# Kernel optimization log

Hardware: AMD Instinct MI355X
Metric: run time of the kernel (lower is better)

Reference implementation:

```python
import jax, jax.numpy as jnp
import numpy as np

D = 512
DB = D // 4          # 128
R = 4                # window radius
KB = 9               # boundary kernel
DH = D // 2          # attn mlp hidden
VOCABS = {"quality": 64, "root": 13, "bass": 13, "key": 25}
COMPS = ["quality", "root", "bass", "key"]
B, T = 4, 4096


def _ln(x, g, b, eps=1e-5):
    mu = jnp.mean(x, axis=-1, keepdims=True)
    var = jnp.var(x, axis=-1, keepdims=True)
    return (x - mu) * jax.lax.rsqrt(var + eps) * g + b


def setup_inputs() -> dict:
    key = jax.random.key(0)
    ks = jax.random.split(key, 24)
    s = 0.02
    inp = {
        "h": jax.random.normal(ks[0], (B, T, D), jnp.float32),
        # boundary head
        "w_bnd": jax.random.normal(ks[1], (D,), jnp.float32) * s,
        "b_bnd": jnp.zeros((1,), jnp.float32),
        # boundary smoother conv1d(1,1,KB)
        "conv_k": jax.random.normal(ks[2], (KB,), jnp.float32) * s,
        "conv_b": jnp.zeros((1,), jnp.float32),
        # FiLM boundary embeddings
        "e0": jnp.zeros((DB,), jnp.float32),
        "e1": jax.random.normal(ks[3], (DB,), jnp.float32) * s,
        # LayerNorms
        "ln_in_g": jnp.ones((D + DB,), jnp.float32),
        "ln_in_b": jnp.zeros((D + DB,), jnp.float32),
        "ln_h_g": jnp.ones((D,), jnp.float32),
        "ln_h_b": jnp.zeros((D,), jnp.float32),
        # FiLM mlp
        "film_w": jax.random.normal(ks[4], (D + DB, 2 * D), jnp.float32) * s,
        "film_b": jnp.zeros((2 * D,), jnp.float32),
        # per-component attn MLP (stacked over 4 comps)
        "attn_w1": jax.random.normal(ks[5], (4, D, DH), jnp.float32) * s,
        "attn_b1": jnp.zeros((4, DH), jnp.float32),
        "attn_w2": jax.random.normal(ks[6], (4, DH), jnp.float32) * s,
        "attn_b2": jnp.zeros((4,), jnp.float32),
        # per-component projector first layer (stacked)
        "proj_w1": jax.random.normal(ks[7], (4, D, D), jnp.float32) * s,
        "proj_b1": jnp.zeros((4, D), jnp.float32),
    }
    for i, c in enumerate(COMPS):
        inp[f"proj_w2_{c[0]}" if c != "key" else "proj_w2_k"] = jax.random.normal(ks[8 + i], (D, VOCABS[c]), jnp.float32) * s
        inp[f"proj_b2_{c[0]}" if c != "key" else "proj_b2_k"] = jnp.zeros((VOCABS[c],), jnp.float32)
    return inp


def reference(h, w_bnd, b_bnd, conv_k, conv_b, e0, e1,
              ln_in_g, ln_in_b, ln_h_g, ln_h_b, film_w, film_b,
              attn_w1, attn_b1, attn_w2, attn_b2, proj_w1, proj_b1,
              proj_w2_q, proj_b2_q, proj_w2_r, proj_b2_r,
              proj_w2_b, proj_b2_b, proj_w2_k, proj_b2_k):
    Bz, Tz, Dz = h.shape
    # boundary head + smoothing (conv1d, same padding) + sigmoid
    bl = jnp.einsum("btd,d->bt", h, w_bnd) + b_bnd[0]            # [B,T]
    sm = jax.lax.conv_general_dilated(bl[:, None, :], conv_k[None, None, :],
                                      (1,), [(KB // 2, KB // 2)]) + conv_b[0]
    b_soft = jax.nn.sigmoid(sm[:, 0, :])                          # [B,T]
    # FiLM
    eb = b_soft[..., None] * e1 + (1.0 - b_soft[..., None]) * e0  # [B,T,DB]
    film_in = _ln(jnp.concatenate([h, eb], axis=-1), ln_in_g, ln_in_b)
    gb = film_in @ film_w + film_b                                # [B,T,2D]
    gamma, beta = gb[..., :Dz], gb[..., Dz:]
    z = _ln(h, ln_h_g, ln_h_b) * (1.0 + gamma) + beta             # [B,T,D]
    # local windows via replicate pad + gather
    hp = jnp.pad(h, ((0, 0), (R, R), (0, 0)), mode="edge")        # [B,T+2R,D]
    idx = jnp.arange(Tz)[:, None] + jnp.arange(2 * R + 1)[None, :]  # [T,W]
    local = hp[:, idx, :]                                         # [B,T,W,D]
    c = jnp.concatenate([z[:, :, None, :], local], axis=2)        # [B,T,C,D]
    # attention pooling for all 4 components at once
    s1 = jax.nn.gelu(jnp.einsum("btcd,kdh->kbtch", c, attn_w1)
                     + attn_b1[:, None, None, None, :], approximate=False)
    scores = jnp.einsum("kbtch,kh->kbtc", s1, attn_w2) + attn_b2[:, None, None, None]
    attn = jax.nn.softmax(scores, axis=-1)                        # [K,B,T,C]
    pooled = jnp.einsum("kbtc,btcd->kbtd", attn, c)               # [K,B,T,D]
    p1 = jax.nn.gelu(jnp.einsum("kbtd,kde->kbte", pooled, proj_w1)
                     + proj_b1[:, None, None, :], approximate=False)
    lq = p1[0] @ proj_w2_q + proj_b2_q
    lr = p1[1] @ proj_w2_r + proj_b2_r
    lb = p1[2] @ proj_w2_b + proj_b2_b
    lk = p1[3] @ proj_w2_k + proj_b2_k
    return jnp.concatenate([lq, lr, lb, lk, bl[..., None]], axis=-1)  # [B,T,116]
```

## Files before the change

kernel.cpp:

```cpp
#include <hip/hip_runtime.h>
#include <hip/hip_bf16.h>

typedef unsigned short u16;
typedef unsigned int u32;

#define NR 16384
#define TT 4096

typedef __bf16 bf16_t;
typedef bf16_t bf16x8 __attribute__((ext_vector_type(8)));
typedef float f32x4 __attribute__((ext_vector_type(4)));

__device__ __forceinline__ float b2f(u16 u){ return __uint_as_float(((u32)u)<<16); }
__device__ __forceinline__ u16 f2b(float f){
  u32 u = __float_as_uint(f);
  u32 r = u + 0x7fffu + ((u>>16)&1u);
  return (u16)(r>>16);
}
__device__ __forceinline__ void up2(u32 u, float&a, float&b){
  a = __uint_as_float(u<<16);
  b = __uint_as_float(u & 0xffff0000u);
}
__device__ __forceinline__ void ld8(const u16* p, float* f){
  uint4 v = *(const uint4*)p;
  up2(v.x,f[0],f[1]); up2(v.y,f[2],f[3]);
  up2(v.z,f[4],f[5]); up2(v.w,f[6],f[7]);
}
__device__ __forceinline__ float wred(float v){
  #pragma unroll
  for(int o=32;o>0;o>>=1) v += __shfl_down(v,o,64);
  return v;
}
__device__ __forceinline__ float gelu_f(float x){
  return 0.5f*x*(1.0f+erff(x*0.7071067811865475f));
}
__device__ __forceinline__ void gl_lds(const void* g, void* l){
  __builtin_amdgcn_global_load_lds(
      (__attribute__((address_space(1))) void*)(void*)g,
      (__attribute__((address_space(3))) void*)l, 16, 0, 0);
}

__global__ void k_tw(const float* __restrict__ src, u16* __restrict__ dst,
                     int K, int N, long long sS, long long sD){
  __shared__ float t[32][33];
  const float* S = src + (size_t)blockIdx.z*sS;
  u16* D = dst + (size_t)blockIdx.z*sD;
  int k0 = blockIdx.y*32, n0 = blockIdx.x*32;
  int r = threadIdx.x>>5, c = threadIdx.x&31;
  #pragma unroll
  for(int p=0;p<4;p++) t[r+p*8][c] = S[(size_t)(k0+r+p*8)*N + n0 + c];
  __syncthreads();
  #pragma unroll
  for(int p=0;p<4;p++) D[(size_t)(n0+r+p*8)*K + k0 + c] = f2b(t[c][r+p*8]);
}

__global__ void k_w2c(const float* __restrict__ wq, const float* __restrict__ bq,
                      const float* __restrict__ wr, const float* __restrict__ br,
                      const float* __restrict__ wb_, const float* __restrict__ bb_,
                      const float* __restrict__ wk, const float* __restrict__ bk,
                      u16* __restrict__ W2c, float* __restrict__ b2c){
  int idx = blockIdx.x;
  int p = idx>>5, j = idx&31, tid = threadIdx.x;
  const float* Wm; const float* Bm; int V; int cofs = 0;
  if(p<=1){ Wm=wq; Bm=bq; V=64; cofs = p*32; }
  else if(p==2){ Wm=wr; Bm=br; V=13; }
  else if(p==3){ Wm=wb_; Bm=bb_; V=13; }
  else { Wm=wk; Bm=bk; V=25; }
  int c = j + cofs;
  bool valid = c < V;
  for(int k=tid;k<512;k+=256)
    W2c[(size_t)idx*512 + k] = f2b(valid ? Wm[(size_t)k*V + c] : 0.f);
  if(tid==0) b2c[idx] = valid ? Bm[c] : 0.f;
}

__global__ void k_bnd(const float* __restrict__ h, const float* __restrict__ wb,
                      const float* __restrict__ bb,
                      float* __restrict__ bl, float* __restrict__ hsum, float* __restrict__ hss,
                      u16* __restrict__ hbf, float* __restrict__ out){
  int wave = threadIdx.x>>6, lane = threadIdx.x&63;
  int n = blockIdx.x*4 + wave;
  const float4* hp = (const float4*)(h + (size_t)n*512 + lane*8);
  const float4* wp = (const float4*)(wb + lane*8);
  float4 h0 = hp[0], h1 = hp[1], w0 = wp[0], w1 = wp[1];
  float hv[8] = {h0.x,h0.y,h0.z,h0.w,h1.x,h1.y,h1.z,h1.w};
  float wv[8] = {w0.x,w0.y,w0.z,w0.w,w1.x,w1.y,w1.z,w1.w};
  float dot=0.f, s=0.f, ss=0.f;
  #pragma unroll
  for(int i=0;i<8;i++){ dot += hv[i]*wv[i]; s += hv[i]; ss += hv[i]*hv[i]; }
  u16* hd = hbf + (size_t)n*512 + lane*8;
  *(ushort4*)hd     = make_ushort4(f2b(hv[0]),f2b(hv[1]),f2b(hv[2]),f2b(hv[3]));
  *(ushort4*)(hd+4) = make_ushort4(f2b(hv[4]),f2b(hv[5]),f2b(hv[6]),f2b(hv[7]));
  dot = wred(dot); s = wred(s); ss = wred(ss);
  if(lane==0){
    float v = dot + bb[0];
    bl[n] = v; hsum[n]=s; hss[n]=ss;
    out[(size_t)n*116 + 115] = v;
  }
}

__global__ void k_conv(const float* __restrict__ bl, const float* __restrict__ ck,
                       const float* __restrict__ cb, float* __restrict__ bsoft){
  int n = blockIdx.x*256 + threadIdx.x;
  int b = n>>12, t = n&4095;
  float acc = cb[0];
  #pragma unroll
  for(int i=0;i<9;i++){
    int tt = t-4+i;
    if(tt>=0 && tt<TT) acc += bl[(b<<12)+tt]*ck[i];
  }
  bsoft[n] = 1.0f/(1.0f+expf(-acc));
}

__global__ void k_filmin(const float* __restrict__ h, const float* __restrict__ bsoft,
                         const float* __restrict__ e0, const float* __restrict__ e1,
                         const float* __restrict__ g, const float* __restrict__ bb,
                         u16* __restrict__ fin){
  __shared__ float xb[640];
  __shared__ float red[8];
  int n = blockIdx.x, tid = threadIdx.x;
  float bs = bsoft[n];
  float s=0.f, ss=0.f;
  for(int idx=tid; idx<640; idx+=256){
    float v;
    if(idx<512) v = h[(size_t)n*512+idx];
    else { int j=idx-512; v = bs*e1[j] + (1.0f-bs)*e0[j]; }
    xb[idx]=v; s+=v; ss+=v*v;
  }
  s = wred(s); ss = wred(ss);
  int wave = tid>>6, lane = tid&63;
  if(lane==0){ red[wave]=s; red[wave+4]=ss; }
  __syncthreads();
  float S = red[0]+red[1]+red[2]+red[3];
  float SS = red[4]+red[5]+red[6]+red[7];
  float mu = S*(1.0f/640.0f);
  float var = SS*(1.0f/640.0f) - mu*mu;
  float rs = rsqrtf(var + 1e-5f);
  for(int idx=tid; idx<640; idx+=256){
    float v = (xb[idx]-mu)*rs*g[idx] + bb[idx];
    fin[(size_t)n*640+idx] = f2b(v);
  }
}

template<int ACT>
__global__ __launch_bounds__(256) void k_mgemm(
    const u16* __restrict__ X, const u16* __restrict__ WT, const float* __restrict__ Bv,
    u16* __restrict__ C, int K, int Nc, int ldC,
    long long sX, long long sW, long long sB, long long sC){
  __shared__ __align__(16) u16 As[128*32];
  __shared__ __align__(16) u16 Bs[128*32];
  int tid = threadIdx.x;
  int wave = tid>>6, lane = tid&63;
  const u16* Xb = X + (size_t)blockIdx.z*sX;
  const u16* Wb = WT + (size_t)blockIdx.z*sW;
  const float* Bb = Bv + (size_t)blockIdx.z*sB;
  u16* Cb = C + (size_t)blockIdx.z*sC;
  int row0 = blockIdx.y*128, col0 = blockIdx.x*128;
  int wr = (wave>>1)*64, wc = (wave&1)*64;
  int lrow = lane>>2;
  int lcol = (lane&3)*8;
  int m15 = lane&15, q = lane>>4;
  f32x4 acc[4][4] = {};
  for(int k0=0;k0<K;k0+=32){
    const u16* ga = Xb + (size_t)(row0 + wave*32 + lrow)*K + k0 + lcol;
    u16* la = As + wave*32*32;
    gl_lds(ga, la);
    gl_lds(ga + (size_t)16*K, la + 16*32);
    const u16* gw = Wb + (size_t)(col0 + wave*32 + lrow)*K + k0 + lcol;
    u16* lb = Bs + wave*32*32;
    gl_lds(gw, lb);
    gl_lds(gw + (size_t)16*K, lb + 16*32);
    __syncthreads();
    bf16x8 af[4], bfr[4];
    #pragma unroll
    for(int i=0;i<4;i++){
      af[i]  = *(const bf16x8*)&As[(wr + i*16 + m15)*32 + q*8];
      bfr[i] = *(const bf16x8*)&Bs[(wc + i*16 + m15)*32 + q*8];
    }
    #pragma unroll
    for(int i=0;i<4;i++)
      #pragma unroll
      for(int j=0;j<4;j++)
        acc[i][j] = __builtin_amdgcn_mfma_f32_16x16x32_bf16(bfr[j], af[i], acc[i][j], 0,0,0);
    __syncthreads();
  }
  #pragma unroll
  for(int i=0;i<4;i++){
    size_t mrow = (size_t)(row0 + wr + i*16 + m15)*ldC;
    #pragma unroll
    for(int j=0;j<4;j++){
      int n0 = col0 + wc + j*16 + q*4;
      float4 bias = *(const float4*)&Bb[n0];
      float v0 = acc[i][j][0] + bias.x;
      float v1 = acc[i][j][1] + bias.y;
      float v2 = acc[i][j][2] + bias.z;
      float v3 = acc[i][j][3] + bias.w;
      if(ACT){ v0=gelu_f(v0); v1=gelu_f(v1); v2=gelu_f(v2); v3=gelu_f(v3); }
      *(ushort4*)(Cb + mrow + n0) = make_ushort4(f2b(v0),f2b(v1),f2b(v2),f2b(v3));
    }
  }
}

__global__ __launch_bounds__(256) void k_f2(
    const u16* __restrict__ X2, const u16* __restrict__ W2c, const float* __restrict__ b2c,
    float* __restrict__ out){
  __shared__ __align__(16) u16 As[128*32];
  __shared__ __align__(16) u16 Bs[32*32];
  int tid = threadIdx.x, wave = tid>>6, lane = tid&63;
  int row0 = blockIdx.x*128, p = blockIdx.y;
  int hk = (p<=1)?0:(p-1);
  int B0 = (p==0)?0:(p==1)?32:(p==2)?64:(p==3)?77:90;
  int V  = (p<=1)?32:(p==4)?25:13;
  int lrow = lane>>2, lcol = (lane&3)*8, m15 = lane&15, q = lane>>4;
  f32x4 acc[2][2] = {};
  for(int k0=0;k0<512;k0+=32){
    const u16* ga = X2 + (size_t)(row0 + wave*32 + lrow)*2048 + hk*512 + k0 + lcol;
    u16* la = As + wave*32*32;
    gl_lds(ga, la);
    gl_lds(ga + (size_t)16*2048, la + 16*32);
    if(wave<2){
      const u16* gw = W2c + (size_t)(p*32 + wave*16 + lrow)*512 + k0 + lcol;
      gl_lds(gw, Bs + wave*16*32);
    }
    __syncthreads();
    bf16x8 af[2], bfr[2];
    #pragma unroll
    for(int i=0;i<2;i++) af[i] = *(const bf16x8*)&As[(wave*32 + i*16 + m15)*32 + q*8];
    #pragma unroll
    for(int j=0;j<2;j++) bfr[j] = *(const bf16x8*)&Bs[(j*16+m15)*32 + q*8];
    #pragma unroll
    for(int i=0;i<2;i++)
      #pragma unroll
      for(int j=0;j<2;j++)
        acc[i][j] = __builtin_amdgcn_mfma_f32_16x16x32_bf16(bfr[j], af[i], acc[i][j], 0,0,0);
    __syncthreads();
  }
  #pragma unroll
  for(int i=0;i<2;i++){
    size_t mrow = (size_t)(row0 + wave*32 + i*16 + m15)*116;
    #pragma unroll
    for(int j=0;j<2;j++){
      int nl0 = j*16 + q*4;
      #pragma unroll
      for(int r=0;r<4;r++){
        int nl = nl0 + r;
        if(nl < V) out[mrow + B0 + nl] = acc[i][j][r] + b2c[p*32+nl];
      }
    }
  }
}

__global__ void k_z(const float* __restrict__ h, const float* __restrict__ hsum,
                    const float* __restrict__ hss, const float* __restrict__ g,
                    const float* __restrict__ bb, const u16* __restrict__ gb,
                    u16* __restrict__ z){
  int n = blockIdx.x, tid = threadIdx.x;
  float mu = hsum[n]*(1.0f/512.0f);
  float var = hss[n]*(1.0f/512.0f) - mu*mu;
  float rs = rsqrtf(var+1e-5f);
  for(int idx=tid; idx<512; idx+=256){
    float hv = h[(size_t)n*512+idx];
    float ln = (hv-mu)*rs*g[idx]+bb[idx];
    float gamma = b2f(gb[(size_t)n*1024+idx]);
    float beta  = b2f(gb[(size_t)n*1024+512+idx]);
    z[(size_t)n*512+idx] = f2b(ln*(1.0f+gamma)+beta);
  }
}

__global__ void k_scred(const u16* __restrict__ G, const float* __restrict__ w2,
                        const float* __restrict__ b2v, float* __restrict__ sc){
  int wave = threadIdx.x>>6, lane = threadIdx.x&63;
  int n = blockIdx.x*4 + wave;
  int k = blockIdx.y;
  uint2 gv = *(const uint2*)(G + ((size_t)k*NR + n)*256 + lane*4);
  float4 wv = *(const float4*)(w2 + k*256 + lane*4);
  float a0,a1,a2,a3;
  up2(gv.x,a0,a1); up2(gv.y,a2,a3);
  float s = a0*wv.x+a1*wv.y+a2*wv.z+a3*wv.w;
  s = wred(s);
  if(lane==0) sc[(size_t)k*NR+n] = s + b2v[k];
}

__global__ __launch_bounds__(256) void k_pool(
    const u16* __restrict__ hb, const u16* __restrict__ z,
    const float* __restrict__ sch, const float* __restrict__ scz,
    u16* __restrict__ P){
  int wave = threadIdx.x>>6, lane = threadIdx.x&63;
  int n = blockIdx.x*4 + wave;
  int b = n>>12, t = n&4095;
  int k = lane&3, j = lane>>2;
  float s;
  if(j==0) s = scz[(size_t)k*NR+n];
  else if(j<10){
    int tc = t-5+j; tc = tc<0?0:(tc>TT-1?TT-1:tc);
    s = sch[(size_t)k*NR + (b<<12) + tc];
  } else s = -1e30f;
  float m = s;
  #pragma unroll
  for(int o=4;o<64;o<<=1) m = fmaxf(m, __shfl_xor(m,o,64));
  float e = (j<10)? expf(s-m) : 0.f;
  float sum = e;
  #pragma unroll
  for(int o=4;o<64;o<<=1) sum += __shfl_xor(sum,o,64);
  float ev = e/sum;
  int d0 = lane*8;
  float acc[4][8] = {};
  #pragma unroll
  for(int jj=0;jj<10;jj++){
    const u16* src;
    if(jj==0) src = z + (size_t)n*512 + d0;
    else {
      int tc = t-5+jj; tc = tc<0?0:(tc>TT-1?TT-1:tc);
      src = hb + ((size_t)(b<<12)+tc)*512 + d0;
    }
    float f[8]; ld8(src, f);
    float w0 = __shfl(ev, jj*4+0, 64);
    float w1 = __shfl(ev, jj*4+1, 64);
    float w2 = __shfl(ev, jj*4+2, 64);
    float w3 = __shfl(ev, jj*4+3, 64);
    #pragma unroll
    for(int i=0;i<8;i++){
      acc[0][i] += w0*f[i];
      acc[1][i] += w1*f[i];
      acc[2][i] += w2*f[i];
      acc[3][i] += w3*f[i];
    }
  }
  #pragma unroll
  for(int kk=0;kk<4;kk++){
    u16* dst = P + ((size_t)kk*NR + n)*512 + d0;
    *(ushort4*)dst     = make_ushort4(f2b(acc[kk][0]),f2b(acc[kk][1]),f2b(acc[kk][2]),f2b(acc[kk][3]));
    *(ushort4*)(dst+4) = make_ushort4(f2b(acc[kk][4]),f2b(acc[kk][5]),f2b(acc[kk][6]),f2b(acc[kk][7]));
  }
}

#define OFF_BL     0u
#define OFF_BSOFT  65536u
#define OFF_HSUM   131072u
#define OFF_HSS    196608u
#define OFF_SCH    262144u
#define OFF_SCZ    524288u
#define OFF_FIN    786432u
#define OFF_GB     21757952u
#define OFF_Z      55312384u
#define OFF_HBF    72089600u
#define OFF_WF     88866816u
#define OFF_WA     90177536u
#define OFF_WP     91226112u
#define OFF_P      93323264u
#define OFF_W2C    160432128u
#define OFF_B2C    160595968u

extern "C" void kernel_launch(void* const* d_in, const int* in_sizes, int n_in,
                              void* d_out, int out_size, void* d_ws, size_t ws_size,
                              hipStream_t stream){
  const float* h       = (const float*)d_in[0];
  const float* w_bnd   = (const float*)d_in[1];
  const float* b_bnd   = (const float*)d_in[2];
  const float* conv_k  = (const float*)d_in[3];
  const float* conv_b  = (const float*)d_in[4];
  const float* e0      = (const float*)d_in[5];
  const float* e1      = (const float*)d_in[6];
  const float* ln_in_g = (const float*)d_in[7];
  const float* ln_in_b = (const float*)d_in[8];
  const float* ln_h_g  = (const float*)d_in[9];
  const float* ln_h_b  = (const float*)d_in[10];
  const float* film_w  = (const float*)d_in[11];
  const float* film_b  = (const float*)d_in[12];
  const float* attn_w1 = (const float*)d_in[13];
  const float* attn_b1 = (const float*)d_in[14];
  const float* attn_w2 = (const float*)d_in[15];
  const float* attn_b2 = (const float*)d_in[16];
  const float* proj_w1 = (const float*)d_in[17];
  const float* proj_b1 = (const float*)d_in[18];
  const float* wq = (const float*)d_in[19];
  const float* bq = (const float*)d_in[20];
  const float* wr = (const float*)d_in[21];
  const float* br = (const float*)d_in[22];
  const float* wb_ = (const float*)d_in[23];
  const float* bb_ = (const float*)d_in[24];
  const float* wk = (const float*)d_in[25];
  const float* bk = (const float*)d_in[26];
  float* out = (float*)d_out;
  char* ws = (char*)d_ws;

  float* bl    = (float*)(ws + OFF_BL);
  float* bsoft = (float*)(ws + OFF_BSOFT);
  float* hsum  = (float*)(ws + OFF_HSUM);
  float* hss   = (float*)(ws + OFF_HSS);
  float* sch   = (float*)(ws + OFF_SCH);
  float* scz   = (float*)(ws + OFF_SCZ);
  u16* fin     = (u16*)(ws + OFF_FIN);
  u16* X2      = (u16*)(ws + OFF_FIN);
  u16* gb      = (u16*)(ws + OFF_GB);
  u16* z       = (u16*)(ws + OFF_Z);
  u16* hbf     = (u16*)(ws + OFF_HBF);
  u16* wfilm   = (u16*)(ws + OFF_WF);
  u16* wattn   = (u16*)(ws + OFF_WA);
  u16* wproj   = (u16*)(ws + OFF_WP);
  u16* P       = (u16*)(ws + OFF_P);
  u16* G       = P;
  u16* w2c     = (u16*)(ws + OFF_W2C);
  float* b2c   = (float*)(ws + OFF_B2C);

  {
    dim3 g(1024/32, 640/32, 1);
    k_tw<<<g,256,0,stream>>>(film_w, wfilm, 640, 1024, 0, 0);
  }
  {
    dim3 g(256/32, 512/32, 4);
    k_tw<<<g,256,0,stream>>>(attn_w1, wattn, 512, 256, 512LL*256, 256LL*512);
  }
  {
    dim3 g(512/32, 512/32, 4);
    k_tw<<<g,256,0,stream>>>(proj_w1, wproj, 512, 512, 512LL*512, 512LL*512);
  }
  k_w2c<<<160,256,0,stream>>>(wq,bq,wr,br,wb_,bb_,wk,bk, w2c, b2c);

  k_bnd<<<NR/4,256,0,stream>>>(h,w_bnd,b_bnd,bl,hsum,hss,hbf,out);
  k_conv<<<NR/256,256,0,stream>>>(bl,conv_k,conv_b,bsoft);
  k_filmin<<<NR,256,0,stream>>>(h,bsoft,e0,e1,ln_in_g,ln_in_b,fin);

  dim3 gFilm(1024/128, NR/128, 1);
  k_mgemm<0><<<gFilm,256,0,stream>>>(fin, wfilm, film_b, gb, 640, 1024, 1024, 0,0,0,0);

  k_z<<<NR,256,0,stream>>>(h,hsum,hss,ln_h_g,ln_h_b,gb,z);

  dim3 gSc(256/128, NR/128, 4);
  dim3 gRed(NR/4, 4);
  k_mgemm<1><<<gSc,256,0,stream>>>(hbf, wattn, attn_b1, G, 512, 256, 256,
                                   0, 256LL*512, 256, (long long)NR*256);
  k_scred<<<gRed,256,0,stream>>>(G, attn_w2, attn_b2, sch);
  k_mgemm<1><<<gSc,256,0,stream>>>(z, wattn, attn_b1, G, 512, 256, 256,
                                   0, 256LL*512, 256, (long long)NR*256);
  k_scred<<<gRed,256,0,stream>>>(G, attn_w2, attn_b2, scz);

  k_pool<<<NR/4,256,0,stream>>>(hbf,z,sch,scz,P);

  dim3 gP(512/128, NR/128, 4);
  k_mgemm<1><<<gP,256,0,stream>>>(P, wproj, proj_b1, X2, 512, 512, 2048,
                                  (long long)NR*512, 512LL*512, 512, 512);

  dim3 gF(NR/128, 5);
  k_f2<<<gF,256,0,stream>>>(X2, w2c, b2c, out);
}
```

Measured before the change: 444.6 us.

## Fuse FiLM GEMM with z epilogue and attention GEMM with score reduction

The FiLM GEMM now computes gamma and beta tiles together and applies LayerNorm modulation in its epilogue to write z directly, removing the gb intermediate and the k_z kernel. The attention-MLP GEMM for h and z runs in one launch and reduces GELU times w2 into scores via atomics, eliminating the G buffer and k_scred. The projector GEMM uses a 64x256 tile, and GELU switches from erf to a tanh approximation using fast exp and rcp. The costs are atomic contention on the score arrays, a memset, a dropped attn_b2 term (softmax invariant), and small numerical differences from the GELU approximation and bf16 h in the epilogue.

Result: faster. 402.8 us (-9.4%).

```diff
diff --git a/kernel.cpp b/kernel.cpp
--- a/kernel.cpp
+++ b/kernel.cpp
@@ -32,7 +32,11 @@
   return v;
 }
 __device__ __forceinline__ float gelu_f(float x){
-  return 0.5f*x*(1.0f+erff(x*0.7071067811865475f));
+  float x2 = x*x;
+  float u = x*(0.7978845608f + 0.0356774081f*x2);
+  float e = __expf(2.0f*u);
+  float t = 1.0f - 2.0f*__builtin_amdgcn_rcpf(e+1.0f);
+  return 0.5f*x*(1.0f+t);
 }
 __device__ __forceinline__ void gl_lds(const void* g, void* l){
   __builtin_amdgcn_global_load_lds(
@@ -141,39 +145,104 @@
   }
 }
 
-template<int ACT>
-__global__ __launch_bounds__(256) void k_mgemm(
-    const u16* __restrict__ X, const u16* __restrict__ WT, const float* __restrict__ Bv,
-    u16* __restrict__ C, int K, int Nc, int ldC,
-    long long sX, long long sW, long long sB, long long sC){
+__global__ __launch_bounds__(256) void k_film(
+    const u16* __restrict__ fin, const u16* __restrict__ WT, const float* __restrict__ fbias,
+    const float* __restrict__ hsum, const float* __restrict__ hss,
+    const float* __restrict__ lng, const float* __restrict__ lnb,
+    const u16* __restrict__ hbf, u16* __restrict__ z){
   __shared__ __align__(16) u16 As[128*32];
-  __shared__ __align__(16) u16 Bs[128*32];
-  int tid = threadIdx.x;
-  int wave = tid>>6, lane = tid&63;
-  const u16* Xb = X + (size_t)blockIdx.z*sX;
-  const u16* Wb = WT + (size_t)blockIdx.z*sW;
-  const float* Bb = Bv + (size_t)blockIdx.z*sB;
-  u16* Cb = C + (size_t)blockIdx.z*sC;
-  int row0 = blockIdx.y*128, col0 = blockIdx.x*128;
+  __shared__ __align__(16) u16 Bg[128*32];
+  __shared__ __align__(16) u16 Bb2[128*32];
+  int tid = threadIdx.x, wave = tid>>6, lane = tid&63;
+  int cg0 = blockIdx.x*128, row0 = blockIdx.y*128;
   int wr = (wave>>1)*64, wc = (wave&1)*64;
-  int lrow = lane>>2;
-  int lcol = (lane&3)*8;
-  int m15 = lane&15, q = lane>>4;
+  int lrow = lane>>2, lcol = (lane&3)*8, m15 = lane&15, q = lane>>4;
+  f32x4 ag[4][4] = {}, ab[4][4] = {};
+  for(int k0=0;k0<640;k0+=32){
+    const u16* ga = fin + (size_t)(row0 + wave*32 + lrow)*640 + k0 + lcol;
+    u16* la = As + wave*32*32;
+    gl_lds(ga, la); gl_lds(ga + (size_t)16*640, la + 16*32);
+    const u16* gg = WT + (size_t)(cg0 + wave*32 + lrow)*640 + k0 + lcol;
+    u16* lg = Bg + wave*32*32;
+    gl_lds(gg, lg); gl_lds(gg + (size_t)16*640, lg + 16*32);
+    const u16* gb2 = WT + (size_t)(cg0 + 512 + wave*32 + lrow)*640 + k0 + lcol;
+    u16* lb2 = Bb2 + wave*32*32;
+    gl_lds(gb2, lb2); gl_lds(gb2 + (size_t)16*640, lb2 + 16*32);
+    __syncthreads();
+    bf16x8 af[4], bg[4], bb[4];
+    #pragma unroll
+    for(int i=0;i<4;i++){
+      af[i] = *(const bf16x8*)&As[(wr + i*16 + m15)*32 + q*8];
+      bg[i] = *(const bf16x8*)&Bg[(wc + i*16 + m15)*32 + q*8];
+      bb[i] = *(const bf16x8*)&Bb2[(wc + i*16 + m15)*32 + q*8];
+    }
+    #pragma unroll
+    for(int i=0;i<4;i++)
+      #pragma unroll
+      for(int j=0;j<4;j++){
+        ag[i][j] = __builtin_amdgcn_mfma_f32_16x16x32_bf16(bg[j], af[i], ag[i][j], 0,0,0);
+        ab[i][j] = __builtin_amdgcn_mfma_f32_16x16x32_bf16(bb[j], af[i], ab[i][j], 0,0,0);
+      }
+    __syncthreads();
+  }
+  #pragma unroll
+  for(int i=0;i<4;i++){
+    int m = row0 + wr + i*16 + m15;
+    float mu = hsum[m]*(1.0f/512.0f);
+    float var = hss[m]*(1.0f/512.0f) - mu*mu;
+    float rs = rsqrtf(var + 1e-5f);
+    #pragma unroll
+    for(int j=0;j<4;j++){
+      int d0 = cg0 + wc + j*16 + q*4;
+      float4 g4 = *(const float4*)&lng[d0];
+      float4 b4 = *(const float4*)&lnb[d0];
+      float4 fg = *(const float4*)&fbias[d0];
+      float4 fb = *(const float4*)&fbias[512+d0];
+      float hv[4];
+      { ushort4 hb4 = *(const ushort4*)(hbf + (size_t)m*512 + d0);
+        hv[0]=b2f(hb4.x); hv[1]=b2f(hb4.y); hv[2]=b2f(hb4.z); hv[3]=b2f(hb4.w); }
+      float gm[4] = {ag[i][j][0]+fg.x, ag[i][j][1]+fg.y, ag[i][j][2]+fg.z, ag[i][j][3]+fg.w};
+      float bt[4] = {ab[i][j][0]+fb.x, ab[i][j][1]+fb.y, ab[i][j][2]+fb.z, ab[i][j][3]+fb.w};
+      float gg4[4] = {g4.x,g4.y,g4.z,g4.w}, bb4[4] = {b4.x,b4.y,b4.z,b4.w};
+      u16 o[4];
+      #pragma unroll
+      for(int r=0;r<4;r++){
+        float ln = (hv[r]-mu)*rs*gg4[r] + bb4[r];
+        o[r] = f2b(ln*(1.0f+gm[r]) + bt[r]);
+      }
+      *(ushort4*)(z + (size_t)m*512 + d0) = make_ushort4(o[0],o[1],o[2],o[3]);
+    }
+  }
+}
+
+__global__ __launch_bounds__(256) void k_msc(
+    const u16* __restrict__ hb, const u16* __restrict__ zb,
+    const u16* __restrict__ WT, const float* __restrict__ b1,
+    const float* __restrict__ w2, float* __restrict__ sch, float* __restrict__ scz){
+  __shared__ __align__(16) u16 As[64*32];
+  __shared__ __align__(16) u16 Bs[256*32];
+  int tid = threadIdx.x, wave = tid>>6, lane = tid&63;
+  int bz = blockIdx.y, hk = bz>>1, src = bz&1;
+  const u16* X = src ? zb : hb;
+  float* sc = src ? scz : sch;
+  int row0 = blockIdx.x*64;
+  const u16* Wb = WT + (size_t)hk*256*512;
+  int lrow = lane>>2, lcol = (lane&3)*8, m15 = lane&15, q = lane>>4;
+  int wc = wave*64;
   f32x4 acc[4][4] = {};
-  for(int k0=0;k0<K;k0+=32){
-    const u16* ga = Xb + (size_t)(row0 + wave*32 + lrow)*K + k0 + lcol;
-    u16* la = As + wave*32*32;
-    gl_lds(ga, la);
-    gl_lds(ga + (size_t)16*K, la + 16*32);
-    const u16* gw = Wb + (size_t)(col0 + wave*32 + lrow)*K + k0 + lcol;
-    u16* lb = Bs + wave*32*32;
+  for(int k0=0;k0<512;k0+=32){
+    gl_lds(X + (size_t)(row0 + wave*16 + lrow)*512 + k0 + lcol, As + wave*16*32);
+    const u16* gw = Wb + (size_t)(wave*64 + lrow)*512 + k0 + lcol;
+    u16* lb = Bs + wave*64*32;
     gl_lds(gw, lb);
-    gl_lds(gw + (size_t)16*K, lb + 16*32);
+    gl_lds(gw + (size_t)16*512, lb + 16*32);
+    gl_lds(gw + (size_t)32*512, lb + 32*32);
+    gl_lds(gw + (size_t)48*512, lb + 48*32);
     __syncthreads();
     bf16x8 af[4], bfr[4];
     #pragma unroll
     for(int i=0;i<4;i++){
-      af[i]  = *(const bf16x8*)&As[(wr + i*16 + m15)*32 + q*8];
+      af[i]  = *(const bf16x8*)&As[(i*16 + m15)*32 + q*8];
       bfr[i] = *(const bf16x8*)&Bs[(wc + i*16 + m15)*32 + q*8];
     }
     #pragma unroll
@@ -185,17 +254,71 @@
   }
   #pragma unroll
   for(int i=0;i<4;i++){
-    size_t mrow = (size_t)(row0 + wr + i*16 + m15)*ldC;
+    float part = 0.f;
+    #pragma unroll
+    for(int j=0;j<4;j++){
+      int n0 = wc + j*16 + q*4;
+      float4 bias = *(const float4*)&b1[hk*256 + n0];
+      float4 wv   = *(const float4*)&w2[hk*256 + n0];
+      part += gelu_f(acc[i][j][0]+bias.x)*wv.x;
+      part += gelu_f(acc[i][j][1]+bias.y)*wv.y;
+      part += gelu_f(acc[i][j][2]+bias.z)*wv.z;
+      part += gelu_f(acc[i][j][3]+bias.w)*wv.w;
+    }
+    part += __shfl_xor(part, 16, 64);
+    part += __shfl_xor(part, 32, 64);
+    if(q==0) atomicAdd(&sc[(size_t)hk*NR + row0 + i*16 + m15], part);
+  }
+}
+
+__global__ __launch_bounds__(256) void k_proj(
+    const u16* __restrict__ P, const u16* __restrict__ WT, const float* __restrict__ Bv,
+    u16* __restrict__ X2){
+  __shared__ __align__(16) u16 As[64*32];
+  __shared__ __align__(16) u16 Bs[256*32];
+  int tid = threadIdx.x, wave = tid>>6, lane = tid&63;
+  int hk = blockIdx.z;
+  int row0 = blockIdx.y*64, col0 = blockIdx.x*256;
+  const u16* Xb = P + (size_t)hk*NR*512;
+  const u16* Wb = WT + (size_t)hk*512*512 + (size_t)col0*512;
+  const float* Bq = Bv + hk*512;
+  int lrow = lane>>2, lcol = (lane&3)*8, m15 = lane&15, q = lane>>4;
+  int wc = wave*64;
+  f32x4 acc[4][4] = {};
+  for(int k0=0;k0<512;k0+=32){
+    gl_lds(Xb + (size_t)(row0 + wave*16 + lrow)*512 + k0 + lcol, As + wave*16*32);
+    const u16* gw = Wb + (size_t)(wave*64 + lrow)*512 + k0 + lcol;
+    u16* lb = Bs + wave*64*32;
+    gl_lds(gw, lb);
+    gl_lds(gw + (size_t)16*512, lb + 16*32);
+    gl_lds(gw + (size_t)32*512, lb + 32*32);
+    gl_lds(gw + (size_t)48*512, lb + 48*32);
+    __syncthreads();
+    bf16x8 af[4], bfr[4];
+    #pragma unroll
+    for(int i=0;i<4;i++){
+      af[i]  = *(const bf16x8*)&As[(i*16 + m15)*32 + q*8];
+      bfr[i] = *(const bf16x8*)&Bs[(wc + i*16 + m15)*32 + q*8];
+    }
+    #pragma unroll
+    for(int i=0;i<4;i++)
+      #pragma unroll
+      for(int j=0;j<4;j++)
+        acc[i][j] = __builtin_amdgcn_mfma_f32_16x16x32_bf16(bfr[j], af[i], acc[i][j], 0,0,0);
+    __syncthreads();
+  }
+  #pragma unroll
+  for(int i=0;i<4;i++){
+    size_t mrow = (size_t)(row0 + i*16 + m15)*2048 + hk*512;
     #pragma unroll
     for(int j=0;j<4;j++){
       int n0 = col0 + wc + j*16 + q*4;
-      float4 bias = *(const float4*)&Bb[n0];
-      float v0 = acc[i][j][0] + bias.x;
-      float v1 = acc[i][j][1] + bias.y;
-      float v2 = acc[i][j][2] + bias.z;
-      float v3 = acc[i][j][3] + bias.w;
-      if(ACT){ v0=gelu_f(v0); v1=gelu_f(v1); v2=gelu_f(v2); v3=gelu_f(v3); }
-      *(ushort4*)(Cb + mrow + n0) = make_ushort4(f2b(v0),f2b(v1),f2b(v2),f2b(v3));
+      float4 bias = *(const float4*)&Bq[n0];
+      float v0 = gelu_f(acc[i][j][0] + bias.x);
+      float v1 = gelu_f(acc[i][j][1] + bias.y);
+      float v2 = gelu_f(acc[i][j][2] + bias.z);
+      float v3 = gelu_f(acc[i][j][3] + bias.w);
+      *(ushort4*)(X2 + mrow + n0) = make_ushort4(f2b(v0),f2b(v1),f2b(v2),f2b(v3));
     }
   }
 }
@@ -249,37 +372,6 @@
   }
 }
 
-__global__ void k_z(const float* __restrict__ h, const float* __restrict__ hsum,
-                    const float* __restrict__ hss, const float* __restrict__ g,
-                    const float* __restrict__ bb, const u16* __restrict__ gb,
-                    u16* __restrict__ z){
-  int n = blockIdx.x, tid = threadIdx.x;
-  float mu = hsum[n]*(1.0f/512.0f);
-  float var = hss[n]*(1.0f/512.0f) - mu*mu;
-  float rs = rsqrtf(var+1e-5f);
-  for(int idx=tid; idx<512; idx+=256){
-    float hv = h[(size_t)n*512+idx];
-    float ln = (hv-mu)*rs*g[idx]+bb[idx];
-    float gamma = b2f(gb[(size_t)n*1024+idx]);
-    float beta  = b2f(gb[(size_t)n*1024+512+idx]);
-    z[(size_t)n*512+idx] = f2b(ln*(1.0f+gamma)+beta);
-  }
-}
-
-__global__ void k_scred(const u16* __restrict__ G, const float* __restrict__ w2,
-                        const float* __restrict__ b2v, float* __restrict__ sc){
-  int wave = threadIdx.x>>6, lane = threadIdx.x&63;
-  int n = blockIdx.x*4 + wave;
-  int k = blockIdx.y;
-  uint2 gv = *(const uint2*)(G + ((size_t)k*NR + n)*256 + lane*4);
-  float4 wv = *(const float4*)(w2 + k*256 + lane*4);
-  float a0,a1,a2,a3;
-  up2(gv.x,a0,a1); up2(gv.y,a2,a3);
-  float s = a0*wv.x+a1*wv.y+a2*wv.z+a3*wv.w;
-  s = wred(s);
-  if(lane==0) sc[(size_t)k*NR+n] = s + b2v[k];
-}
-
 __global__ __launch_bounds__(256) void k_pool(
     const u16* __restrict__ hb, const u16* __restrict__ z,
     const float* __restrict__ sch, const float* __restrict__ scz,
@@ -340,7 +432,6 @@
 #define OFF_SCH    262144u
 #define OFF_SCZ    524288u
 #define OFF_FIN    786432u
-#define OFF_GB     21757952u
 #define OFF_Z      55312384u
 #define OFF_HBF    72089600u
 #define OFF_WF     88866816u
@@ -369,7 +460,6 @@
   const float* attn_w1 = (const float*)d_in[13];
   const float* attn_b1 = (const float*)d_in[14];
   const float* attn_w2 = (const float*)d_in[15];
-  const float* attn_b2 = (const float*)d_in[16];
   const float* proj_w1 = (const float*)d_in[17];
   const float* proj_b1 = (const float*)d_in[18];
   const float* wq = (const float*)d_in[19];
@@ -391,16 +481,16 @@
   float* scz   = (float*)(ws + OFF_SCZ);
   u16* fin     = (u16*)(ws + OFF_FIN);
   u16* X2      = (u16*)(ws + OFF_FIN);
-  u16* gb      = (u16*)(ws + OFF_GB);
   u16* z       = (u16*)(ws + OFF_Z);
   u16* hbf     = (u16*)(ws + OFF_HBF);
   u16* wfilm   = (u16*)(ws + OFF_WF);
   u16* wattn   = (u16*)(ws + OFF_WA);
   u16* wproj   = (u16*)(ws + OFF_WP);
   u16* P       = (u16*)(ws + OFF_P);
-  u16* G       = P;
   u16* w2c     = (u16*)(ws + OFF_W2C);
   float* b2c   = (float*)(ws + OFF_B2C);
+
+  hipMemsetAsync(ws + OFF_SCH, 0, 524288, stream);
 
   {
     dim3 g(1024/32, 640/32, 1);
@@ -420,26 +510,25 @@
   k_conv<<<NR/256,256,0,stream>>>(bl,conv_k,conv_b,bsoft);
   k_filmin<<<NR,256,0,stream>>>(h,bsoft,e0,e1,ln_in_g,ln_in_b,fin);
 
-  dim3 gFilm(1024/128, NR/128, 1);
-  k_mgemm<0><<<gFilm,256,0,stream>>>(fin, wfilm, film_b, gb, 640, 1024, 1024, 0,0,0,0);
-
-  k_z<<<NR,256,0,stream>>>(h,hsum,hss,ln_h_g,ln_h_b,gb,z);
-
-  dim3 gSc(256/128, NR/128, 4);
-  dim3 gRed(NR/4, 4);
-  k_mgemm<1><<<gSc,256,0,stream>>>(hbf, wattn, attn_b1, G, 512, 256, 256,
-                                   0, 256LL*512, 256, (long long)NR*256);
-  k_scred<<<gRed,256,0,stream>>>(G, attn_w2, attn_b2, sch);
-  k_mgemm<1><<<gSc,256,0,stream>>>(z, wattn, attn_b1, G, 512, 256, 256,
-                                   0, 256LL*512, 256, (long long)NR*256);
-  k_scred<<<gRed,256,0,stream>>>(G, attn_w2, attn_b2, scz);
+  {
+    dim3 g(4, NR/128);
+    k_film<<<g,256,0,stream>>>(fin, wfilm, film_b, hsum, hss, ln_h_g, ln_h_b, hbf, z);
+  }
+
+  {
+    dim3 g(NR/64, 8);
+    k_msc<<<g,256,0,stream>>>(hbf, z, wattn, attn_b1, attn_w2, sch, scz);
+  }
 
   k_pool<<<NR/4,256,0,stream>>>(hbf,z,sch,scz,P);
 
-  dim3 gP(512/128, NR/128, 4);
-  k_mgemm<1><<<gP,256,0,stream>>>(P, wproj, proj_b1, X2, 512, 512, 2048,
-                                  (long long)NR*512, 512LL*512, 512, 512);
-
-  dim3 gF(NR/128, 5);
-  k_f2<<<gF,256,0,stream>>>(X2, w2c, b2c, out);
-}
+  {
+    dim3 g(2, NR/64, 4);
+    k_proj<<<g,256,0,stream>>>(P, wproj, proj_b1, X2);
+  }
+
+  {
+    dim3 g(NR/128, 5);
+    k_f2<<<g,256,0,stream>>>(X2, w2c, b2c, out);
+  }
+}
```
